# Performance work log

Hardware: AMD Instinct MI355X
Metric: run time of the kernel (lower is better)

Reference implementation:

```python
import jax, jax.numpy as jnp
import numpy as np

E = 256  # embed_dim == input_chn (required by ln_ff broadcast)
B = 256
LAMBDA_INIT = float(0.8 - 0.6 * np.exp(-0.3 * 1.0))  # layer_index = 1


def rmsnorm(x, scale, d, eps=1e-8):
    # matches torch RMSNorm: rms = ||x||_2 / sqrt(d); x / (rms + eps) * scale
    norm = jnp.linalg.norm(x, axis=-1, keepdims=True)
    rms = norm * (d ** -0.5)
    return scale * (x / (rms + eps))


def setup_inputs() -> dict:
    key = jax.random.key(0)
    ks = jax.random.split(key, 12)
    x = jax.random.normal(ks[0], (B, E, E), jnp.float32)
    s = 0.02
    return {
        "x": x,
        "Wq": jax.random.normal(ks[1], (E, 2 * E), jnp.float32) * s,
        "bq": jnp.zeros((2 * E,), jnp.float32),
        "Wk": jax.random.normal(ks[2], (E, 2 * E), jnp.float32) * s,
        "bk": jnp.zeros((2 * E,), jnp.float32),
        "Wv": jax.random.normal(ks[3], (E, E), jnp.float32) * s,
        "bv": jnp.zeros((E,), jnp.float32),
        "lq1": jax.random.normal(ks[4], (E,), jnp.float32) * 0.1,
        "lk1": jax.random.normal(ks[5], (E,), jnp.float32) * 0.1,
        "lq2": jax.random.normal(ks[6], (E,), jnp.float32) * 0.1,
        "lk2": jax.random.normal(ks[7], (E,), jnp.float32) * 0.1,
        "ln_attn_scale": jnp.ones((E,), jnp.float32),
        "norm_scale": jnp.ones((E,), jnp.float32),
        "ln_ff_scale": jnp.ones((E,), jnp.float32),
        "W1": jax.random.normal(ks[8], (E, 4 * E), jnp.float32) * s,
        "b1": jnp.zeros((4 * E,), jnp.float32),
        "W2": jax.random.normal(ks[9], (4 * E, E), jnp.float32) * s,
        "b2": jnp.zeros((E,), jnp.float32),
    }


def reference(x, Wq, bq, Wk, bk, Wv, bv, lq1, lk1, lq2, lk2,
              ln_attn_scale, norm_scale, ln_ff_scale, W1, b1, W2, b2):
    scale = E ** -0.25
    # a = ln_attn(x^T)^T  (normalize over seq dim which equals E)
    a = jnp.swapaxes(rmsnorm(jnp.swapaxes(x, -1, -2), ln_attn_scale, E), -1, -2)
    # decompose: moving average kernel=5, stride=1, edge-replicate padding 2 on seq dim
    ap = jnp.pad(a, ((0, 0), (2, 2), (0, 0)), mode="edge")
    trend = (ap[:, 0:-4] + ap[:, 1:-3] + ap[:, 2:-2] + ap[:, 3:-1] + ap[:, 4:]) / 5.0
    seasonal = a - trend
    # Q from trend, K from seasonal, V from a; all projected along the seq(=E) dim
    q = jnp.swapaxes(trend, -1, -2) @ Wq + bq          # [B, C, 2E]
    q1, q2 = jnp.split(q, 2, axis=-1)
    k = jnp.swapaxes(seasonal, -1, -2) @ Wk + bk       # [B, C, 2E]
    k1, k2 = jnp.split(k, 2, axis=-1)
    v = jnp.swapaxes(a, -1, -2) @ Wv + bv              # [B, C, E]
    a1 = jnp.einsum("bce,bde->bcd", q1, k1) * scale    # [B, C, C]
    a2 = jnp.einsum("bce,bde->bcd", q2, k2) * scale
    lam = jnp.exp(jnp.sum(lq1 * lk1)) - jnp.exp(jnp.sum(lq2 * lk2)) + LAMBDA_INIT
    d = jax.nn.softmax(a1, axis=-1) - lam * jax.nn.softmax(a2, axis=-1)
    attn = rmsnorm(d @ v, norm_scale, E) * (1.0 - LAMBDA_INIT)  # [B, C, E]
    x = x + jnp.swapaxes(attn, -1, -2)
    # FFN branch: ln_ff over last dim (chn == E), then project along seq dim
    h = jnp.swapaxes(rmsnorm(x, ln_ff_scale, E), -1, -2)        # [B, C, E]
    h = jax.nn.silu(h @ W1 + b1) @ W2 + b2                      # [B, C, E]
    x = x + jnp.swapaxes(h, -1, -2)
    return x
```

## Files before the change

kernel.cpp:

```cpp
#include <hip/hip_runtime.h>
#include <math.h>

static constexpr int E = 256;
static constexpr int BTOT = 256;

typedef __bf16 bf16;
typedef __bf16 bf16x8 __attribute__((ext_vector_type(8)));
typedef __bf16 bf16x4 __attribute__((ext_vector_type(4)));
typedef float f32x4 __attribute__((ext_vector_type(4)));

__device__ __forceinline__ void gload16(const void* g, void* l) {
  __builtin_amdgcn_global_load_lds(
      (const __attribute__((address_space(1))) void*)g,
      (__attribute__((address_space(3))) void*)l, 16, 0, 0);
}

__device__ __forceinline__ void xcd_decode(int b, int NX, int nPanels, int& x, int& g) {
  if ((nPanels & 7) == 0) {
    int gLo = b & 7;
    int t2 = b >> 3;
    x = t2 % NX;
    g = (t2 / NX) * 8 + gLo;
  } else {
    x = b % NX;
    g = b / NX;
  }
}

__device__ __forceinline__ float fsig(float x) {
  return __fdividef(1.0f, 1.0f + __expf(-x));
}

__global__ __launch_bounds__(256) void k_wT(const float* __restrict__ src,
                                            bf16* __restrict__ dst, int R, int C) {
  __shared__ float lds[32][33];
  int tiles_c = C >> 5;
  int tc = blockIdx.x % tiles_c;
  int tr = blockIdx.x / tiles_c;
  int r0 = tr << 5, c0 = tc << 5;
  int t = threadIdx.x, cc = t & 31, rr0 = t >> 5;
#pragma unroll
  for (int p = 0; p < 4; ++p) {
    int rr = rr0 + p * 8;
    lds[rr][cc] = src[(size_t)(r0 + rr) * C + (c0 + cc)];
  }
  __syncthreads();
#pragma unroll
  for (int p = 0; p < 4; ++p) {
    int rr = rr0 + p * 8;
    dst[(size_t)(c0 + rr) * R + (r0 + cc)] = (bf16)lds[cc][rr];
  }
}

__global__ void k_lam(const float* lq1, const float* lk1, const float* lq2,
                      const float* lk2, float lambda_init, float* lamOut) {
  int t = threadIdx.x;
  float v1 = lq1[t] * lk1[t];
  float v2 = lq2[t] * lk2[t];
  __shared__ float s1[4], s2[4];
#pragma unroll
  for (int o = 32; o; o >>= 1) { v1 += __shfl_xor(v1, o); v2 += __shfl_xor(v2, o); }
  if ((t & 63) == 0) { s1[t >> 6] = v1; s2[t >> 6] = v2; }
  __syncthreads();
  if (t == 0) {
    float a = s1[0] + s1[1] + s1[2] + s1[3];
    float b = s2[0] + s2[1] + s2[2] + s2[3];
    *lamOut = expf(a) - expf(b) + lambda_init;
  }
}

__global__ __launch_bounds__(1024) void k_rmsA(const float* __restrict__ x, int batchBase,
                                               float* __restrict__ rinvA) {
  __shared__ float red[4][257];
  int lz = blockIdx.x;
  int g = batchBase + lz;
  int t = threadIdx.x, j = t & 255, qd = t >> 8;
  const float* xb = x + (size_t)g * E * E;
  float s = 0.f;
#pragma unroll 4
  for (int ii = 0; ii < 64; ++ii) {
    float v = xb[(size_t)(qd * 64 + ii) * E + j];
    s += v * v;
  }
  red[qd][j] = s;
  __syncthreads();
  if (qd == 0) {
    float tot = red[0][j] + red[1][j] + red[2][j] + red[3][j];
    rinvA[lz * E + j] = __fdividef(1.0f, sqrtf(tot) * 0.0625f + 1e-8f);
  }
}

__global__ __launch_bounds__(256) void k_prep(const float* __restrict__ x, int batchBase,
                                              const float* __restrict__ rinvA,
                                              const float* __restrict__ lnattn,
                                              bf16* __restrict__ a_t,
                                              bf16* __restrict__ tr_t, bf16* __restrict__ se_t) {
  __shared__ float lA[36][261];
  int lz = blockIdx.y, g = batchBase + lz;
  int i0 = blockIdx.x << 5;
  int t = threadIdx.x;
  const float* xb = x + (size_t)g * E * E;
  float rj = rinvA[lz * E + t];
#pragma unroll
  for (int rr = 0; rr < 36; ++rr) {
    int gi = i0 - 2 + rr;
    gi = gi < 0 ? 0 : (gi > 255 ? 255 : gi);
    float v = xb[(size_t)gi * E + t];
    lA[rr][t] = lnattn[gi] * v * rj;
  }
  __syncthreads();
  size_t bo = (size_t)lz * E * E;
  int ic = t & 31, jg = t >> 5;
#pragma unroll 4
  for (int jj = 0; jj < 32; ++jj) {
    int j = jg + jj * 8;
    float a0 = lA[ic][j], a1 = lA[ic + 1][j], a2 = lA[ic + 2][j];
    float a3 = lA[ic + 3][j], a4 = lA[ic + 4][j];
    float tr = (a0 + a1 + a2 + a3 + a4) * 0.2f;
    size_t o = bo + (size_t)j * E + i0 + ic;
    a_t[o] = (bf16)a2;
    tr_t[o] = (bf16)tr;
    se_t[o] = (bf16)(a2 - tr);
  }
}

template <int EPI>
__global__ __launch_bounds__(256) void gemm_bt(
    const bf16* __restrict__ A, int lda, size_t aStride,
    const bf16* __restrict__ B, int ldb, size_t bStride,
    bf16* __restrict__ Out, int ldo, size_t oStride, int K,
    const float* __restrict__ biasN, const float* __restrict__ biasM,
    int NX, int NY, int nPanels) {
  __shared__ __align__(128) bf16 As[128][64];
  __shared__ __align__(128) bf16 Bs[128][64];
  int xdec, gdec;
  xcd_decode(blockIdx.x, NX, nPanels, xdec, gdec);
  int lz = gdec / NY;
  int mb = (gdec % NY) << 7, nb = xdec << 7;
  const bf16* Ab = A + (size_t)lz * aStride;
  const bf16* Bb = B + (size_t)lz * bStride;
  int t = threadIdx.x, lane = t & 63, wv = t >> 6;
  int wr = wv >> 1, wc = wv & 1;
  int lrow = lane >> 3;
  int kel = ((lane & 7) ^ lrow) << 3;
  f32x4 acc[4][4];
  const f32x4 z4 = {0.f, 0.f, 0.f, 0.f};
#pragma unroll
  for (int a = 0; a < 4; ++a)
#pragma unroll
    for (int b = 0; b < 4; ++b) acc[a][b] = z4;
  for (int k0 = 0; k0 < K; k0 += 64) {
    __syncthreads();
#pragma unroll
    for (int i = 0; i < 4; ++i) {
      int rb = i * 32 + wv * 8;
      gload16(&Ab[(size_t)(mb + rb + lrow) * lda + k0 + kel], &As[rb][0]);
      gload16(&Bb[(size_t)(nb + rb + lrow) * ldb + k0 + kel], &Bs[rb][0]);
    }
    __syncthreads();
#pragma unroll
    for (int kk = 0; kk < 2; ++kk) {
      int kb = (kk * 64 + ((lane >> 4) << 4)) ^ ((lane & 7) << 4);
      bf16x8 af[4], bfr[4];
#pragma unroll
      for (int mi = 0; mi < 4; ++mi)
        af[mi] = *(const bf16x8*)((const char*)As + (wr * 64 + mi * 16 + (lane & 15)) * 128 + kb);
#pragma unroll
      for (int ni = 0; ni < 4; ++ni)
        bfr[ni] = *(const bf16x8*)((const char*)Bs + (wc * 64 + ni * 16 + (lane & 15)) * 128 + kb);
#pragma unroll
      for (int mi = 0; mi < 4; ++mi)
#pragma unroll
        for (int ni = 0; ni < 4; ++ni)
          acc[mi][ni] = __builtin_amdgcn_mfma_f32_16x16x32_bf16(af[mi], bfr[ni],
                                                                acc[mi][ni], 0, 0, 0);
    }
  }
  int colB = nb + wc * 64 + (lane & 15);
  int rowB = mb + wr * 64 + ((lane >> 4) << 2);
#pragma unroll
  for (int mi = 0; mi < 4; ++mi) {
#pragma unroll
    for (int ni = 0; ni < 4; ++ni) {
      int col = colB + ni * 16;
      float bN = 0.f;
      if constexpr (EPI == 1) bN = biasN[col];
#pragma unroll
      for (int r = 0; r < 4; ++r) {
        int row = rowB + mi * 16 + r;
        float v = acc[mi][ni][r];
        if constexpr (EPI == 1) {
          Out[(size_t)lz * oStride + (size_t)row * ldo + col] = (bf16)(v + bN);
        } else {
          Out[(size_t)lz * oStride + (size_t)row * ldo + col] = (bf16)(v + biasM[row]);
        }
      }
    }
  }
}

__global__ __launch_bounds__(512) void k_score(const bf16* __restrict__ q,
                                               const bf16* __restrict__ km,
                                               const float* __restrict__ lamPtr,
                                               bf16* __restrict__ D, int nPanels) {
  __shared__ __align__(128) bf16 As[128][64];
  __shared__ __align__(128) bf16 Bs[256][64];
  __shared__ float red[4][128];
  int xdec, lz;
  xcd_decode(blockIdx.x, 2, nPanels, xdec, lz);
  int mb = xdec << 7;
  const bf16* qb = q + (size_t)lz * E * 512;
  const bf16* kb = km + (size_t)lz * E * 512;
  int t = threadIdx.x, lane = t & 63, wv = t >> 6;
  int wr = wv >> 2, wc = wv & 3;
  int lrow = lane >> 3;
  int kel = ((lane & 7) ^ lrow) << 3;
  f32x4 acc1[4][4], acc2[4][4];
  const f32x4 z4 = {0.f, 0.f, 0.f, 0.f};
#pragma unroll
  for (int a = 0; a < 4; ++a)
#pragma unroll
    for (int b = 0; b < 4; ++b) { acc1[a][b] = z4; acc2[a][b] = z4; }
#pragma unroll
  for (int mat = 0; mat < 2; ++mat) {
    f32x4(*acc)[4] = mat == 0 ? acc1 : acc2;
    const bf16* qm = qb + mat * 256;
    const bf16* kmm = kb + mat * 256;
    for (int k0 = 0; k0 < 256; k0 += 64) {
      __syncthreads();
#pragma unroll
      for (int i = 0; i < 2; ++i) {
        int rb = i * 64 + wv * 8;
        gload16(&qm[(size_t)(mb + rb + lrow) * 512 + k0 + kel], &As[rb][0]);
      }
#pragma unroll
      for (int i = 0; i < 4; ++i) {
        int rb = i * 64 + wv * 8;
        gload16(&kmm[(size_t)(rb + lrow) * 512 + k0 + kel], &Bs[rb][0]);
      }
      __syncthreads();
#pragma unroll
      for (int kk = 0; kk < 2; ++kk) {
        int kb2 = (kk * 64 + ((lane >> 4) << 4)) ^ ((lane & 7) << 4);
        bf16x8 af[4], bfr[4];
#pragma unroll
        for (int mi = 0; mi < 4; ++mi)
          af[mi] = *(const bf16x8*)((const char*)As + (wr * 64 + mi * 16 + (lane & 15)) * 128 + kb2);
#pragma unroll
        for (int ni = 0; ni < 4; ++ni)
          bfr[ni] = *(const bf16x8*)((const char*)Bs + (wc * 64 + ni * 16 + (lane & 15)) * 128 + kb2);
#pragma unroll
        for (int mi = 0; mi < 4; ++mi)
#pragma unroll
          for (int ni = 0; ni < 4; ++ni)
            acc[mi][ni] = __builtin_amdgcn_mfma_f32_16x16x32_bf16(af[mi], bfr[ni],
                                                                  acc[mi][ni], 0, 0, 0);
      }
    }
  }
  float lam = *lamPtr;
  int rbase = wr * 64 + ((lane >> 4) << 2);
  float inv1[4][4], inv2[4][4];
  __syncthreads();
#pragma unroll
  for (int mat = 0; mat < 2; ++mat) {
    f32x4(*acc)[4] = mat == 0 ? acc1 : acc2;
    float(*inv)[4] = mat == 0 ? inv1 : inv2;
    float tmp[4][4];
#pragma unroll
    for (int mi = 0; mi < 4; ++mi)
#pragma unroll
      for (int r = 0; r < 4; ++r) {
        float m = fmaxf(fmaxf(acc[mi][0][r], acc[mi][1][r]),
                        fmaxf(acc[mi][2][r], acc[mi][3][r]));
        m = fmaxf(m, __shfl_xor(m, 1));
        m = fmaxf(m, __shfl_xor(m, 2));
        m = fmaxf(m, __shfl_xor(m, 4));
        m = fmaxf(m, __shfl_xor(m, 8));
        tmp[mi][r] = m;
      }
    if ((lane & 15) == 0) {
#pragma unroll
      for (int mi = 0; mi < 4; ++mi)
#pragma unroll
        for (int r = 0; r < 4; ++r) red[wc][rbase + mi * 16 + r] = tmp[mi][r];
    }
    __syncthreads();
#pragma unroll
    for (int mi = 0; mi < 4; ++mi)
#pragma unroll
      for (int r = 0; r < 4; ++r) {
        int rw = rbase + mi * 16 + r;
        tmp[mi][r] = fmaxf(fmaxf(red[0][rw], red[1][rw]), fmaxf(red[2][rw], red[3][rw]));
      }
    __syncthreads();
#pragma unroll
    for (int mi = 0; mi < 4; ++mi)
#pragma unroll
      for (int r = 0; r < 4; ++r) {
        float m = tmp[mi][r], s = 0.f;
#pragma unroll
        for (int ni = 0; ni < 4; ++ni) {
          float p = __expf(0.25f * (acc[mi][ni][r] - m));
          acc[mi][ni][r] = p;
          s += p;
        }
        s += __shfl_xor(s, 1);
        s += __shfl_xor(s, 2);
        s += __shfl_xor(s, 4);
        s += __shfl_xor(s, 8);
        tmp[mi][r] = s;
      }
    if ((lane & 15) == 0) {
#pragma unroll
      for (int mi = 0; mi < 4; ++mi)
#pragma unroll
        for (int r = 0; r < 4; ++r) red[wc][rbase + mi * 16 + r] = tmp[mi][r];
    }
    __syncthreads();
#pragma unroll
    for (int mi = 0; mi < 4; ++mi)
#pragma unroll
      for (int r = 0; r < 4; ++r) {
        int rw = rbase + mi * 16 + r;
        inv[mi][r] = __fdividef(1.0f, red[0][rw] + red[1][rw] + red[2][rw] + red[3][rw]);
      }
    __syncthreads();
  }
  size_t Dbase = (size_t)lz * E * E;
#pragma unroll
  for (int mi = 0; mi < 4; ++mi)
#pragma unroll
    for (int ni = 0; ni < 4; ++ni) {
      int col = wc * 64 + ni * 16 + (lane & 15);
#pragma unroll
      for (int r = 0; r < 4; ++r) {
        int row = mb + rbase + mi * 16 + r;
        D[Dbase + (size_t)row * E + col] =
            (bf16)(acc1[mi][ni][r] * inv1[mi][r] - lam * acc2[mi][ni][r] * inv2[mi][r]);
      }
    }
}

__global__ __launch_bounds__(512) void k_pv(const bf16* __restrict__ Dm,
                                            const bf16* __restrict__ vT,
                                            const float* __restrict__ x, int batchBase,
                                            const float* __restrict__ nscale,
                                            float oml, bf16* __restrict__ Y, int nPanels) {
  __shared__ __align__(128) bf16 As[128][64];
  __shared__ __align__(128) bf16 Bs[256][64];
  __shared__ float red[4][128];
  int xdec, lz;
  xcd_decode(blockIdx.x, 2, nPanels, xdec, lz);
  int mb = xdec << 7;
  const bf16* Ab = Dm + (size_t)lz * E * E;
  const bf16* Bb = vT + (size_t)lz * E * E;
  int t = threadIdx.x, lane = t & 63, wv = t >> 6;
  int wr = wv >> 2, wc = wv & 3;
  int lrow = lane >> 3;
  int kel = ((lane & 7) ^ lrow) << 3;
  f32x4 acc[4][4];
  const f32x4 z4 = {0.f, 0.f, 0.f, 0.f};
#pragma unroll
  for (int a = 0; a < 4; ++a)
#pragma unroll
    for (int b = 0; b < 4; ++b) acc[a][b] = z4;
  for (int k0 = 0; k0 < 256; k0 += 64) {
    __syncthreads();
#pragma unroll
    for (int i = 0; i < 2; ++i) {
      int rb = i * 64 + wv * 8;
      gload16(&Ab[(size_t)(mb + rb + lrow) * E + k0 + kel], &As[rb][0]);
    }
#pragma unroll
    for (int i = 0; i < 4; ++i) {
      int rb = i * 64 + wv * 8;
      gload16(&Bb[(size_t)(rb + lrow) * E + k0 + kel], &Bs[rb][0]);
    }
    __syncthreads();
#pragma unroll
    for (int kk = 0; kk < 2; ++kk) {
      int kb2 = (kk * 64 + ((lane >> 4) << 4)) ^ ((lane & 7) << 4);
      bf16x8 af[4], bfr[4];
#pragma unroll
      for (int mi = 0; mi < 4; ++mi)
        af[mi] = *(const bf16x8*)((const char*)As + (wr * 64 + mi * 16 + (lane & 15)) * 128 + kb2);
#pragma unroll
      for (int ni = 0; ni < 4; ++ni)
        bfr[ni] = *(const bf16x8*)((const char*)Bs + (wc * 64 + ni * 16 + (lane & 15)) * 128 + kb2);
#pragma unroll
      for (int mi = 0; mi < 4; ++mi)
#pragma unroll
        for (int ni = 0; ni < 4; ++ni)
          acc[mi][ni] = __builtin_amdgcn_mfma_f32_16x16x32_bf16(af[mi], bfr[ni],
                                                                acc[mi][ni], 0, 0, 0);
    }
  }
  int rbase = wr * 64 + ((lane >> 4) << 2);
  float rowinv[4][4];
#pragma unroll
  for (int mi = 0; mi < 4; ++mi)
#pragma unroll
    for (int r = 0; r < 4; ++r) {
      float s = 0.f;
#pragma unroll
      for (int ni = 0; ni < 4; ++ni) {
        float v = acc[mi][ni][r];
        s += v * v;
      }
      s += __shfl_xor(s, 1);
      s += __shfl_xor(s, 2);
      s += __shfl_xor(s, 4);
      s += __shfl_xor(s, 8);
      rowinv[mi][r] = s;
    }
  if ((lane & 15) == 0) {
#pragma unroll
    for (int mi = 0; mi < 4; ++mi)
#pragma unroll
      for (int r = 0; r < 4; ++r) red[wc][rbase + mi * 16 + r] = rowinv[mi][r];
  }
  __syncthreads();
#pragma unroll
  for (int mi = 0; mi < 4; ++mi)
#pragma unroll
    for (int r = 0; r < 4; ++r) {
      int rw = rbase + mi * 16 + r;
      float tot = red[0][rw] + red[1][rw] + red[2][rw] + red[3][rw];
      rowinv[mi][r] = oml * __fdividef(1.0f, sqrtf(tot) * 0.0625f + 1e-8f);
    }
  size_t bo = (size_t)lz * E * E;
  const float* xb = x + (size_t)(batchBase + lz) * E * E;
#pragma unroll
  for (int mi = 0; mi < 4; ++mi)
#pragma unroll
    for (int ni = 0; ni < 4; ++ni) {
      int col = wc * 64 + ni * 16 + (lane & 15);
      float ns = nscale[col];
      int row0 = mb + rbase + mi * 16;
      f32x4 xv = *(const f32x4*)&xb[(size_t)col * E + row0];
#pragma unroll
      for (int r = 0; r < 4; ++r) {
        size_t o = bo + (size_t)(row0 + r) * E + col;
        Y[o] = (bf16)(xv[r] + ns * acc[mi][ni][r] * rowinv[mi][r]);
      }
    }
}

__global__ __launch_bounds__(256) void k_ffnorm(const bf16* __restrict__ Y,
                                                const float* __restrict__ lnff,
                                                bf16* __restrict__ xn) {
  __shared__ float red[8][33];
  __shared__ float rl[32];
  int lz = blockIdx.y;
  int i0 = blockIdx.x << 5;
  int t = threadIdx.x, ic = t & 31, jg = t >> 5;
  size_t bo = (size_t)lz * E * E;
  float s = 0.f;
#pragma unroll 4
  for (int jj = 0; jj < 32; ++jj) {
    int j = jg + jj * 8;
    float v = (float)Y[bo + (size_t)j * E + i0 + ic];
    s += v * v;
  }
  red[jg][ic] = s;
  __syncthreads();
  if (jg == 0) {
    float tot = 0.f;
#pragma unroll
    for (int g2 = 0; g2 < 8; ++g2) tot += red[g2][ic];
    rl[ic] = __fdividef(1.0f, sqrtf(tot) * 0.0625f + 1e-8f);
  }
  __syncthreads();
  float rinv = rl[ic];
#pragma unroll 4
  for (int jj = 0; jj < 32; ++jj) {
    int j = jg + jj * 8;
    size_t o = bo + (size_t)j * E + i0 + ic;
    xn[o] = (bf16)(lnff[j] * (float)Y[o] * rinv);
  }
}

__global__ __launch_bounds__(1024) void k_ffn(const bf16* __restrict__ xn,
                                              const bf16* __restrict__ W1T,
                                              const bf16* __restrict__ W2T,
                                              const float* __restrict__ b1,
                                              const float* __restrict__ b2,
                                              const bf16* __restrict__ Y,
                                              int batchBase, float* __restrict__ out) {
  __shared__ __align__(128) char arena[131072];
  char* Hb = arena;
  char* xnL = arena + 32768;
  char* S0 = arena + 65536;
  char* S1 = arena + 98304;
  int bid = blockIdx.x;
  int lz = bid >> 2;
  int c0 = (bid & 3) << 6;
  const bf16* xb = xn + (size_t)lz * E * E + (size_t)c0 * E;
  int t = threadIdx.x, lane = t & 63, wv = t >> 6;
  int lrow = lane >> 3;
  int kel = ((lane & 7) ^ lrow) << 3;
  int l15 = lane & 15, l4 = lane >> 4, l7 = lane & 7;
  int wr1 = wv >> 1, wc1 = wv & 1;
  int wr2 = wv >> 1, wc2 = wv & 1;

  f32x4 b1v4[4][2];
#pragma unroll
  for (int ch = 0; ch < 4; ++ch)
#pragma unroll
    for (int mi = 0; mi < 2; ++mi)
      b1v4[ch][mi] = *(const f32x4*)&b1[ch * 256 + wr1 * 32 + mi * 16 + l4 * 4];

#pragma unroll
  for (int j = 0; j < 2; ++j) {
    int lin = wv * 2 + j;
    int ksub = lin >> 3, rg = (lin & 7) * 8;
    gload16(&xb[(size_t)(rg + lrow) * E + ksub * 64 + kel], xnL + ksub * 8192 + rg * 128);
  }
#pragma unroll
  for (int i = 0; i < 2; ++i) {
    int rb = i * 128 + wv * 8;
    gload16(&W1T[(size_t)(rb + lrow) * 256 + kel], S0 + rb * 128);
  }

  f32x4 acc2[2][2];
  const f32x4 z4 = {0.f, 0.f, 0.f, 0.f};
  acc2[0][0] = z4; acc2[0][1] = z4; acc2[1][0] = z4; acc2[1][1] = z4;
  int cur = 0;

  for (int ch = 0; ch < 4; ++ch) {
    f32x4 acc1[2][2];
    acc1[0][0] = z4; acc1[0][1] = z4; acc1[1][0] = z4; acc1[1][1] = z4;
    for (int k = 0; k < 4; ++k) {
      char* Sn = cur ? S0 : S1;
      if (k < 3) {
#pragma unroll
        for (int i = 0; i < 2; ++i) {
          int rb = i * 128 + wv * 8;
          gload16(&W1T[(size_t)(ch * 256 + rb + lrow) * 256 + (k + 1) * 64 + kel], Sn + rb * 128);
        }
      } else {
#pragma unroll
        for (int i = 0; i < 2; ++i) {
          int rb = i * 128 + wv * 8;
          gload16(&W2T[(size_t)(rb + lrow) * 1024 + ch * 256 + kel], Sn + rb * 128);
        }
      }
      asm volatile("s_waitcnt vmcnt(2)" ::: "memory");
      __builtin_amdgcn_s_barrier();
      char* Sc = cur ? S1 : S0;
      __builtin_amdgcn_s_setprio(1);
#pragma unroll
      for (int kk = 0; kk < 2; ++kk) {
        int kb = (kk * 64 + (l4 << 4)) ^ (l7 << 4);
        bf16x8 af[2], bfr[2];
#pragma unroll
        for (int mi = 0; mi < 2; ++mi)
          af[mi] = *(const bf16x8*)(Sc + (wr1 * 32 + mi * 16 + l15) * 128 + kb);
#pragma unroll
        for (int ni = 0; ni < 2; ++ni)
          bfr[ni] = *(const bf16x8*)(xnL + k * 8192 + (wc1 * 32 + ni * 16 + l15) * 128 + kb);
#pragma unroll
        for (int mi = 0; mi < 2; ++mi)
#pragma unroll
          for (int ni = 0; ni < 2; ++ni)
            acc1[mi][ni] = __builtin_amdgcn_mfma_f32_16x16x32_bf16(af[mi], bfr[ni],
                                                                   acc1[mi][ni], 0, 0, 0);
      }
      __builtin_amdgcn_s_setprio(0);
      __builtin_amdgcn_s_barrier();
      cur ^= 1;
    }
#pragma unroll
    for (int mi = 0; mi < 2; ++mi) {
      int e1b = wr1 * 32 + mi * 16 + l4 * 4;
      f32x4 bN = b1v4[ch][mi];
#pragma unroll
      for (int ni = 0; ni < 2; ++ni) {
        int c = wc1 * 32 + ni * 16 + l15;
        bf16x4 hv;
#pragma unroll
        for (int r = 0; r < 4; ++r) {
          float u = acc1[mi][ni][r] + bN[r];
          hv[r] = (bf16)(u * fsig(u));
        }
        *(bf16x4*)(Hb + c * 512 + ((2 * e1b) ^ ((c & 7) << 4))) = hv;
      }
    }
    asm volatile("s_waitcnt lgkmcnt(0)" ::: "memory");
    for (int k = 0; k < 4; ++k) {
      char* Sn = cur ? S0 : S1;
      bool isLast = (ch == 3) && (k == 3);
      if (k < 3) {
#pragma unroll
        for (int i = 0; i < 2; ++i) {
          int rb = i * 128 + wv * 8;
          gload16(&W2T[(size_t)(rb + lrow) * 1024 + ch * 256 + (k + 1) * 64 + kel], Sn + rb * 128);
        }
      } else if (ch < 3) {
#pragma unroll
        for (int i = 0; i < 2; ++i) {
          int rb = i * 128 + wv * 8;
          gload16(&W1T[(size_t)((ch + 1) * 256 + rb + lrow) * 256 + kel], Sn + rb * 128);
        }
      }
      if (isLast) asm volatile("s_waitcnt vmcnt(0)" ::: "memory");
      else        asm volatile("s_waitcnt vmcnt(2)" ::: "memory");
      __builtin_amdgcn_s_barrier();
      char* Sc = cur ? S1 : S0;
      __builtin_amdgcn_s_setprio(1);
#pragma unroll
      for (int kk = 0; kk < 2; ++kk) {
        int kb = (kk * 64 + (l4 << 4)) ^ (l7 << 4);
        int kbH = (k * 128 + kk * 64 + (l4 << 4)) ^ (l7 << 4);
        bf16x8 af[2], bfr[2];
#pragma unroll
        for (int mi = 0; mi < 2; ++mi)
          af[mi] = *(const bf16x8*)(Sc + (wr2 * 32 + mi * 16 + l15) * 128 + kb);
#pragma unroll
        for (int ni = 0; ni < 2; ++ni)
          bfr[ni] = *(const bf16x8*)(Hb + (wc2 * 32 + ni * 16 + l15) * 512 + kbH);
#pragma unroll
        for (int mi = 0; mi < 2; ++mi)
#pragma unroll
          for (int ni = 0; ni < 2; ++ni)
            acc2[mi][ni] = __builtin_amdgcn_mfma_f32_16x16x32_bf16(af[mi], bfr[ni],
                                                                   acc2[mi][ni], 0, 0, 0);
      }
      __builtin_amdgcn_s_setprio(0);
      __builtin_amdgcn_s_barrier();
      cur ^= 1;
    }
  }
  const bf16* Yb = Y + (size_t)lz * E * E;
  float* ob = out + (size_t)(batchBase + lz) * E * E;
#pragma unroll
  for (int mi = 0; mi < 2; ++mi) {
    int e2b = wr2 * 32 + mi * 16 + l4 * 4;
    f32x4 bv = *(const f32x4*)&b2[e2b];
#pragma unroll
    for (int ni = 0; ni < 2; ++ni) {
      int c = c0 + wc2 * 32 + ni * 16 + l15;
      bf16x4 yv = *(const bf16x4*)&Yb[(size_t)c * E + e2b];
#pragma unroll
      for (int r = 0; r < 4; ++r)
        ob[(size_t)(e2b + r) * E + c] = acc2[mi][ni][r] + bv[r] + (float)yv[r];
    }
  }
}

extern "C" void kernel_launch(void* const* d_in, const int* in_sizes, int n_in,
                              void* d_out, int out_size, void* d_ws, size_t ws_size,
                              hipStream_t stream) {
  const float* x = (const float*)d_in[0];
  const float* Wq = (const float*)d_in[1];
  const float* bq = (const float*)d_in[2];
  const float* Wk = (const float*)d_in[3];
  const float* bk = (const float*)d_in[4];
  const float* Wv = (const float*)d_in[5];
  const float* bv = (const float*)d_in[6];
  const float* lq1 = (const float*)d_in[7];
  const float* lk1 = (const float*)d_in[8];
  const float* lq2 = (const float*)d_in[9];
  const float* lk2 = (const float*)d_in[10];
  const float* lnattn = (const float*)d_in[11];
  const float* nscale = (const float*)d_in[12];
  const float* lnff = (const float*)d_in[13];
  const float* W1 = (const float*)d_in[14];
  const float* b1 = (const float*)d_in[15];
  const float* W2 = (const float*)d_in[16];
  const float* b2 = (const float*)d_in[17];
  float* out = (float*)d_out;

  char* ws = (char*)d_ws;
  size_t off = 0;
  auto alloc = [&](size_t bytes) {
    size_t o = off;
    off += (bytes + 255) & ~(size_t)255;
    return o;
  };
  size_t oWqT = alloc(512 * 256 * 2);
  size_t oWkT = alloc(512 * 256 * 2);
  size_t oWvT = alloc(256 * 256 * 2);
  size_t oW1T = alloc(1024 * 256 * 2);
  size_t oW2T = alloc(256 * 1024 * 2);
  size_t oLam = alloc(256);
  size_t weightEnd = off;

  const size_t szH = (size_t)E * E * 2;
  const size_t szQ = (size_t)E * 512 * 2;
  const size_t szRi = 1024;
  size_t perBatch = 4 * szH + 2 * szQ + szRi;
  size_t avail = ws_size > weightEnd ? ws_size - weightEnd : 0;
  int NB = (int)(avail / perBatch);
  if (NB > BTOT) NB = BTOT;
  if (NB < 1) NB = 1;

  size_t o = weightEnd;
  auto allocN = [&](size_t bytes) {
    size_t r = o;
    o += bytes * (size_t)NB;
    return r;
  };
  bf16* pA = (bf16*)(ws + allocN(szH));
  bf16* pTr = (bf16*)(ws + allocN(szH));
  bf16* pSe = (bf16*)(ws + allocN(szH));
  bf16* pVT = (bf16*)(ws + allocN(szH));
  size_t oQK = allocN(2 * szQ);
  float* pRiA = (float*)(ws + allocN(szRi));

  bf16* pQ = (bf16*)(ws + oQK);
  bf16* pK = (bf16*)(ws + oQK + (size_t)NB * szQ);
  bf16* pD = pTr;
  bf16* pY = pA;
  bf16* pXn = pSe;

  bf16* pWqT = (bf16*)(ws + oWqT);
  bf16* pWkT = (bf16*)(ws + oWkT);
  bf16* pWvT = (bf16*)(ws + oWvT);
  bf16* pW1T = (bf16*)(ws + oW1T);
  bf16* pW2T = (bf16*)(ws + oW2T);
  float* pLam = (float*)(ws + oLam);

  const float LAMBDA_INIT = 0.8f - 0.6f * expf(-0.3f);
  const float OML = 1.0f - LAMBDA_INIT;

  k_wT<<<dim3((256 / 32) * (512 / 32)), 256, 0, stream>>>(Wq, pWqT, 256, 512);
  k_wT<<<dim3((256 / 32) * (512 / 32)), 256, 0, stream>>>(Wk, pWkT, 256, 512);
  k_wT<<<dim3((256 / 32) * (256 / 32)), 256, 0, stream>>>(Wv, pWvT, 256, 256);
  k_wT<<<dim3((256 / 32) * (1024 / 32)), 256, 0, stream>>>(W1, pW1T, 256, 1024);
  k_wT<<<dim3((1024 / 32) * (256 / 32)), 256, 0, stream>>>(W2, pW2T, 1024, 256);
  k_lam<<<1, 256, 0, stream>>>(lq1, lk1, lq2, lk2, LAMBDA_INIT, pLam);

  for (int base = 0; base < BTOT; base += NB) {
    int cnt = BTOT - base < NB ? BTOT - base : NB;
    k_rmsA<<<dim3(cnt), 1024, 0, stream>>>(x, base, pRiA);
    k_prep<<<dim3(8, cnt), 256, 0, stream>>>(x, base, pRiA, lnattn, pA, pTr, pSe);
    gemm_bt<1><<<dim3(4 * 2 * cnt), 256, 0, stream>>>(pTr, 256, 65536, pWqT, 256, 0,
        pQ, 512, 131072, 256, bq, nullptr, 4, 2, 2 * cnt);
    gemm_bt<1><<<dim3(4 * 2 * cnt), 256, 0, stream>>>(pSe, 256, 65536, pWkT, 256, 0,
        pK, 512, 131072, 256, bk, nullptr, 4, 2, 2 * cnt);
    gemm_bt<2><<<dim3(2 * 2 * cnt), 256, 0, stream>>>(pWvT, 256, 0, pA, 256, 65536,
        pVT, 256, 65536, 256, nullptr, bv, 2, 2, 2 * cnt);
    k_score<<<dim3(2 * cnt), 512, 0, stream>>>(pQ, pK, pLam, pD, cnt);
    k_pv<<<dim3(2 * cnt), 512, 0, stream>>>(pD, pVT, x, base, nscale, OML, pY, cnt);
    k_ffnorm<<<dim3(8, cnt), 256, 0, stream>>>(pY, lnff, pXn);
    k_ffn<<<dim3(4 * cnt), 1024, 0, stream>>>(pXn, pW1T, pW2T, b1, b2, pY, base, out);
  }
}
```

Baseline: 532.9 us.

## Restructure fused FFN kernel to 512 threads with register-resident activations

The fused FFN kernel moves from 1024 to 512 threads per block. The hidden dimension is now processed in eight 128-wide chunks instead of four 256-wide ones, which shrinks the hidden-activation buffer and the LDS arena from 128KB to 80KB. The activation tile is kept in registers instead of being staged in LDS. Each wave now computes larger tiles (4x1 for the first GEMM, 4x2 for the second), and b1 is loaded per chunk. The goal is more blocks resident per CU and fewer LDS reads, at the cost of higher register pressure and more barrier phases per block.

```diff
diff --git a/kernel.cpp b/kernel.cpp
--- a/kernel.cpp
+++ b/kernel.cpp
@@ -481,147 +481,144 @@
   }
 }
 
-__global__ __launch_bounds__(1024) void k_ffn(const bf16* __restrict__ xn,
-                                              const bf16* __restrict__ W1T,
-                                              const bf16* __restrict__ W2T,
-                                              const float* __restrict__ b1,
-                                              const float* __restrict__ b2,
-                                              const bf16* __restrict__ Y,
-                                              int batchBase, float* __restrict__ out) {
-  __shared__ __align__(128) char arena[131072];
+__global__ __launch_bounds__(512, 4) void k_ffn(const bf16* __restrict__ xn,
+                                                const bf16* __restrict__ W1T,
+                                                const bf16* __restrict__ W2T,
+                                                const float* __restrict__ b1,
+                                                const float* __restrict__ b2,
+                                                const bf16* __restrict__ Y,
+                                                int batchBase, float* __restrict__ out) {
+  __shared__ __align__(128) char arena[81920];
   char* Hb = arena;
-  char* xnL = arena + 32768;
-  char* S0 = arena + 65536;
-  char* S1 = arena + 98304;
+  char* S0 = arena + 16384;
+  char* S1 = arena + 49152;
   int bid = blockIdx.x;
   int lz = bid >> 2;
   int c0 = (bid & 3) << 6;
-  const bf16* xb = xn + (size_t)lz * E * E + (size_t)c0 * E;
   int t = threadIdx.x, lane = t & 63, wv = t >> 6;
   int lrow = lane >> 3;
   int kel = ((lane & 7) ^ lrow) << 3;
   int l15 = lane & 15, l4 = lane >> 4, l7 = lane & 7;
-  int wr1 = wv >> 1, wc1 = wv & 1;
+  int wr1 = wv >> 2, wc1 = wv & 3;
   int wr2 = wv >> 1, wc2 = wv & 1;
 
-  f32x4 b1v4[4][2];
-#pragma unroll
-  for (int ch = 0; ch < 4; ++ch)
-#pragma unroll
-    for (int mi = 0; mi < 2; ++mi)
-      b1v4[ch][mi] = *(const f32x4*)&b1[ch * 256 + wr1 * 32 + mi * 16 + l4 * 4];
+  const bf16* xg = xn + (size_t)lz * E * E + (size_t)(c0 + wc1 * 16 + l15) * E;
+  bf16x8 xr[4][2];
+#pragma unroll
+  for (int st = 0; st < 4; ++st)
+#pragma unroll
+    for (int kk = 0; kk < 2; ++kk)
+      xr[st][kk] = *(const bf16x8*)&xg[st * 64 + kk * 32 + l4 * 8];
 
 #pragma unroll
   for (int j = 0; j < 2; ++j) {
-    int lin = wv * 2 + j;
-    int ksub = lin >> 3, rg = (lin & 7) * 8;
-    gload16(&xb[(size_t)(rg + lrow) * E + ksub * 64 + kel], xnL + ksub * 8192 + rg * 128);
-  }
-#pragma unroll
-  for (int i = 0; i < 2; ++i) {
-    int rb = i * 128 + wv * 8;
+    int rb = (wv * 2 + j) * 8;
     gload16(&W1T[(size_t)(rb + lrow) * 256 + kel], S0 + rb * 128);
   }
 
-  f32x4 acc2[2][2];
+  f32x4 acc2[4][2];
   const f32x4 z4 = {0.f, 0.f, 0.f, 0.f};
-  acc2[0][0] = z4; acc2[0][1] = z4; acc2[1][0] = z4; acc2[1][1] = z4;
+#pragma unroll
+  for (int a = 0; a < 4; ++a) { acc2[a][0] = z4; acc2[a][1] = z4; }
   int cur = 0;
-
-  for (int ch = 0; ch < 4; ++ch) {
-    f32x4 acc1[2][2];
-    acc1[0][0] = z4; acc1[0][1] = z4; acc1[1][0] = z4; acc1[1][1] = z4;
+  f32x4 b1f[4];
+
+  for (int ch = 0; ch < 8; ++ch) {
+    f32x4 acc1[4];
+#pragma unroll
+    for (int a = 0; a < 4; ++a) acc1[a] = z4;
     for (int k = 0; k < 4; ++k) {
       char* Sn = cur ? S0 : S1;
       if (k < 3) {
 #pragma unroll
-        for (int i = 0; i < 2; ++i) {
-          int rb = i * 128 + wv * 8;
-          gload16(&W1T[(size_t)(ch * 256 + rb + lrow) * 256 + (k + 1) * 64 + kel], Sn + rb * 128);
+        for (int j = 0; j < 2; ++j) {
+          int rb = (wv * 2 + j) * 8;
+          gload16(&W1T[(size_t)(ch * 128 + rb + lrow) * 256 + (k + 1) * 64 + kel],
+                  Sn + rb * 128);
         }
+        asm volatile("s_waitcnt vmcnt(2)" ::: "memory");
       } else {
 #pragma unroll
-        for (int i = 0; i < 2; ++i) {
-          int rb = i * 128 + wv * 8;
-          gload16(&W2T[(size_t)(rb + lrow) * 1024 + ch * 256 + kel], Sn + rb * 128);
+        for (int mi = 0; mi < 4; ++mi)
+          b1f[mi] = *(const f32x4*)&b1[ch * 128 + wr1 * 64 + mi * 16 + l4 * 4];
+#pragma unroll
+        for (int j = 0; j < 4; ++j) {
+          int rb = (wv * 4 + j) * 8;
+          gload16(&W2T[(size_t)(rb + lrow) * 1024 + ch * 128 + kel], Sn + rb * 128);
         }
-      }
-      asm volatile("s_waitcnt vmcnt(2)" ::: "memory");
+        asm volatile("s_waitcnt vmcnt(8)" ::: "memory");
+      }
       __builtin_amdgcn_s_barrier();
       char* Sc = cur ? S1 : S0;
       __builtin_amdgcn_s_setprio(1);
 #pragma unroll
       for (int kk = 0; kk < 2; ++kk) {
         int kb = (kk * 64 + (l4 << 4)) ^ (l7 << 4);
-        bf16x8 af[2], bfr[2];
-#pragma unroll
-        for (int mi = 0; mi < 2; ++mi)
-          af[mi] = *(const bf16x8*)(Sc + (wr1 * 32 + mi * 16 + l15) * 128 + kb);
-#pragma unroll
-        for (int ni = 0; ni < 2; ++ni)
-          bfr[ni] = *(const bf16x8*)(xnL + k * 8192 + (wc1 * 32 + ni * 16 + l15) * 128 + kb);
-#pragma unroll
-        for (int mi = 0; mi < 2; ++mi)
-#pragma unroll
-          for (int ni = 0; ni < 2; ++ni)
-            acc1[mi][ni] = __builtin_amdgcn_mfma_f32_16x16x32_bf16(af[mi], bfr[ni],
-                                                                   acc1[mi][ni], 0, 0, 0);
+        bf16x8 af[4];
+#pragma unroll
+        for (int mi = 0; mi < 4; ++mi)
+          af[mi] = *(const bf16x8*)(Sc + (wr1 * 64 + mi * 16 + l15) * 128 + kb);
+#pragma unroll
+        for (int mi = 0; mi < 4; ++mi)
+          acc1[mi] = __builtin_amdgcn_mfma_f32_16x16x32_bf16(af[mi], xr[k][kk],
+                                                             acc1[mi], 0, 0, 0);
       }
       __builtin_amdgcn_s_setprio(0);
       __builtin_amdgcn_s_barrier();
       cur ^= 1;
     }
-#pragma unroll
-    for (int mi = 0; mi < 2; ++mi) {
-      int e1b = wr1 * 32 + mi * 16 + l4 * 4;
-      f32x4 bN = b1v4[ch][mi];
-#pragma unroll
-      for (int ni = 0; ni < 2; ++ni) {
-        int c = wc1 * 32 + ni * 16 + l15;
+    asm volatile("s_waitcnt vmcnt(4)" ::: "memory");
+    {
+      int c = wc1 * 16 + l15;
+      int sw = (c & 7) << 4;
+#pragma unroll
+      for (int mi = 0; mi < 4; ++mi) {
+        int e1b = wr1 * 64 + mi * 16 + l4 * 4;
         bf16x4 hv;
 #pragma unroll
         for (int r = 0; r < 4; ++r) {
-          float u = acc1[mi][ni][r] + bN[r];
+          float u = acc1[mi][r] + b1f[mi][r];
           hv[r] = (bf16)(u * fsig(u));
         }
-        *(bf16x4*)(Hb + c * 512 + ((2 * e1b) ^ ((c & 7) << 4))) = hv;
+        *(bf16x4*)(Hb + c * 256 + ((2 * e1b) ^ sw)) = hv;
       }
     }
     asm volatile("s_waitcnt lgkmcnt(0)" ::: "memory");
-    for (int k = 0; k < 4; ++k) {
+    for (int k2 = 0; k2 < 2; ++k2) {
       char* Sn = cur ? S0 : S1;
-      bool isLast = (ch == 3) && (k == 3);
-      if (k < 3) {
-#pragma unroll
-        for (int i = 0; i < 2; ++i) {
-          int rb = i * 128 + wv * 8;
-          gload16(&W2T[(size_t)(rb + lrow) * 1024 + ch * 256 + (k + 1) * 64 + kel], Sn + rb * 128);
+      if (k2 == 0) {
+#pragma unroll
+        for (int j = 0; j < 4; ++j) {
+          int rb = (wv * 4 + j) * 8;
+          gload16(&W2T[(size_t)(rb + lrow) * 1024 + ch * 128 + 64 + kel], Sn + rb * 128);
         }
-      } else if (ch < 3) {
-#pragma unroll
-        for (int i = 0; i < 2; ++i) {
-          int rb = i * 128 + wv * 8;
-          gload16(&W1T[(size_t)((ch + 1) * 256 + rb + lrow) * 256 + kel], Sn + rb * 128);
+        asm volatile("s_waitcnt vmcnt(4)" ::: "memory");
+      } else if (ch < 7) {
+#pragma unroll
+        for (int j = 0; j < 2; ++j) {
+          int rb = (wv * 2 + j) * 8;
+          gload16(&W1T[(size_t)((ch + 1) * 128 + rb + lrow) * 256 + kel], Sn + rb * 128);
         }
-      }
-      if (isLast) asm volatile("s_waitcnt vmcnt(0)" ::: "memory");
-      else        asm volatile("s_waitcnt vmcnt(2)" ::: "memory");
+        asm volatile("s_waitcnt vmcnt(2)" ::: "memory");
+      } else {
+        asm volatile("s_waitcnt vmcnt(0)" ::: "memory");
+      }
       __builtin_amdgcn_s_barrier();
       char* Sc = cur ? S1 : S0;
       __builtin_amdgcn_s_setprio(1);
 #pragma unroll
       for (int kk = 0; kk < 2; ++kk) {
         int kb = (kk * 64 + (l4 << 4)) ^ (l7 << 4);
-        int kbH = (k * 128 + kk * 64 + (l4 << 4)) ^ (l7 << 4);
-        bf16x8 af[2], bfr[2];
-#pragma unroll
-        for (int mi = 0; mi < 2; ++mi)
-          af[mi] = *(const bf16x8*)(Sc + (wr2 * 32 + mi * 16 + l15) * 128 + kb);
+        int kbH = (k2 * 128 + kk * 64 + (l4 << 4)) ^ (l7 << 4);
+        bf16x8 af[4], bfr[2];
+#pragma unroll
+        for (int mi = 0; mi < 4; ++mi)
+          af[mi] = *(const bf16x8*)(Sc + (wr2 * 64 + mi * 16 + l15) * 128 + kb);
 #pragma unroll
         for (int ni = 0; ni < 2; ++ni)
-          bfr[ni] = *(const bf16x8*)(Hb + (wc2 * 32 + ni * 16 + l15) * 512 + kbH);
-#pragma unroll
-        for (int mi = 0; mi < 2; ++mi)
+          bfr[ni] = *(const bf16x8*)(Hb + (wc2 * 32 + ni * 16 + l15) * 256 + kbH);
+#pragma unroll
+        for (int mi = 0; mi < 4; ++mi)
 #pragma unroll
           for (int ni = 0; ni < 2; ++ni)
             acc2[mi][ni] = __builtin_amdgcn_mfma_f32_16x16x32_bf16(af[mi], bfr[ni],
@@ -635,8 +632,8 @@
   const bf16* Yb = Y + (size_t)lz * E * E;
   float* ob = out + (size_t)(batchBase + lz) * E * E;
 #pragma unroll
-  for (int mi = 0; mi < 2; ++mi) {
-    int e2b = wr2 * 32 + mi * 16 + l4 * 4;
+  for (int mi = 0; mi < 4; ++mi) {
+    int e2b = wr2 * 64 + mi * 16 + l4 * 4;
     f32x4 bv = *(const f32x4*)&b2[e2b];
 #pragma unroll
     for (int ni = 0; ni < 2; ++ni) {
@@ -745,6 +742,6 @@
     k_score<<<dim3(2 * cnt), 512, 0, stream>>>(pQ, pK, pLam, pD, cnt);
     k_pv<<<dim3(2 * cnt), 512, 0, stream>>>(pD, pVT, x, base, nscale, OML, pY, cnt);
     k_ffnorm<<<dim3(8, cnt), 256, 0, stream>>>(pY, lnff, pXn);
-    k_ffn<<<dim3(4 * cnt), 1024, 0, stream>>>(pXn, pW1T, pW2T, b1, b2, pY, base, out);
-  }
-}
+    k_ffn<<<dim3(4 * cnt), 512, 0, stream>>>(pXn, pW1T, pW2T, b1, b2, pY, base, out);
+  }
+}
```

New measurement: 639.1 us. 19.9% more time.
